# Kernel optimization log

Hardware: AMD Instinct MI355X
Metric: run time of the kernel (lower is better)

## Reference

```python
import jax, jax.numpy as jnp
import numpy as np
import math

NUM_HEADS = 8
HEAD_DIM = 64
SEQ = 128
EPS = 1e-6


def _rel_pos_bucket(rel_pos, num_buckets=32, max_dist=128):
    # bidirectional T5 bucketing
    n = -rel_pos
    num_buckets //= 2  # 16
    ret = (n < 0).astype(jnp.int32) * num_buckets
    n = jnp.abs(n)
    max_exact = num_buckets // 2  # 8
    is_small = n < max_exact
    nf = jnp.maximum(n, 1).astype(jnp.float32)  # guard log(0); masked by is_small
    val_if_large = max_exact + (
        jnp.log(nf / max_exact) / math.log(max_dist / max_exact) * (num_buckets - max_exact)
    ).astype(jnp.int32)
    val_if_large = jnp.minimum(val_if_large, num_buckets - 1)
    return ret + jnp.where(is_small, n, val_if_large)


def setup_inputs() -> dict:
    key = jax.random.key(0)
    ks = jax.random.split(key, 8)
    d = 512
    return {
        "x": jax.random.randint(ks[0], (1, SEQ), 0, 32128),
        "x_len": jax.random.randint(ks[1], (1,), 64, SEQ + 1),
        "embed": jax.random.normal(ks[2], (32128, d), jnp.float32) * 0.02,
        "scale": jnp.ones((d,), jnp.float32),
        "rel_bias_w": jax.random.normal(ks[3], (NUM_HEADS, 32), jnp.float32) * 0.02,
        "qw": jax.random.normal(ks[4], (d, d), jnp.float32) * 0.02,
        "kw": jax.random.normal(ks[5], (d, d), jnp.float32) * 0.02,
        "vw": jax.random.normal(ks[6], (d, d), jnp.float32) * 0.02,
    }


def reference(x, x_len, embed, scale, rel_bias_w, qw, kw, vw):
    B, S = x.shape  # (1, 128)
    H, D = NUM_HEADS, HEAD_DIM

    # embedding gather + RMSNorm + length mask
    h = embed[x]  # [B,S,512]
    var = jnp.mean(jnp.square(h), axis=-1, keepdims=True)
    h = h * jax.lax.rsqrt(var + EPS) * scale
    mask = (jnp.arange(S) < x_len[:, None]).astype(h.dtype)  # [B,S]
    h = h * mask[..., None]

    # relative-position bias gather [H,S,S]
    pos = jnp.arange(S, dtype=jnp.int32)
    rp_bucket = _rel_pos_bucket(pos[:, None] - pos[None, :])  # [S,S]
    rel_bias = rel_bias_w[:, rp_bucket]  # [H,S,S]
    rel_bias = rel_bias + (1.0 - mask[..., None]) * -1e9  # B==1 broadcast

    def split_heads(e):
        # [B,S,512] -> [B*H,S,D]
        return e.reshape(B, S, H, D).transpose(0, 2, 1, 3).reshape(B * H, S, D)

    q = split_heads(h @ qw)
    k = split_heads(h @ kw)
    v = split_heads(h @ vw)

    attn_weights = jnp.einsum("hqd,hkd->hqk", q, k)  # [B*H,S,S]
    attn_weights = attn_weights + jnp.transpose(rel_bias, (0, 2, 1))
    attn_probs = jax.nn.softmax(attn_weights, axis=-1)
    attn_output = jnp.einsum("hqk,hkd->hqd", attn_probs, v)  # [B*H,S,D]
    return (rel_bias, attn_weights, attn_output)
```

## Files before the change

kernel.cpp:

```cpp
#include <hip/hip_runtime.h>

#define SEQL 128
#define DM   512
#define NH   8
#define HD   64

typedef unsigned short ushort_t;
typedef unsigned int   uint_t;
typedef __attribute__((ext_vector_type(8))) __bf16 bf16x8;
typedef __attribute__((ext_vector_type(4))) float  f32x4;

__device__ __forceinline__ ushort_t f2bf(float f) {
    uint_t u = __float_as_uint(f);
    u += 0x7fffu + ((u >> 16) & 1u);
    return (ushort_t)(u >> 16);
}

__device__ __forceinline__ int rel_bucket(int i, int j) {
    int n = j - i;
    int ret = 0;
    if (n < 0) { ret = 16; n = -n; }
    if (n < 8) return ret + n;
    float nf = (float)n;
    int vil = 8 + (int)((logf(nf * 0.125f) / logf(16.0f)) * 8.0f);
    vil = vil < 15 ? vil : 15;
    return ret + vil;
}

__global__ __launch_bounds__(256) void k_qkv_fused(
    const int* __restrict__ x, const int* __restrict__ xlen,
    const float* __restrict__ embed, const float* __restrict__ scale,
    const float* __restrict__ qw, const float* __restrict__ kw,
    const float* __restrict__ vw,
    float* __restrict__ q, float* __restrict__ k, float* __restrict__ v) {
    __shared__ ushort_t Ash[64 * 512];
    __shared__ ushort_t Bsh[2][64 * 64];
    const int t  = threadIdx.x;
    const int n0 = blockIdx.x * 64;
    const int m0 = blockIdx.y * 64;
    const int wi = blockIdx.z;
    const float* __restrict__ W = (wi == 0) ? qw : (wi == 1) ? kw : vw;
    float* __restrict__ O       = (wi == 0) ? q  : (wi == 1) ? k  : v;
    const int xl = xlen[0];

    const int nloc = t & 63, khq = t >> 6;
    const float* __restrict__ wcol = W + n0 + nloc;
    float rc[16];
#pragma unroll
    for (int i = 0; i < 16; ++i) rc[i] = wcol[(size_t)(khq * 16 + i) * DM];

    const int lane7 = t & 7;
#pragma unroll
    for (int p = 0; p < 2; ++p) {
        const int mloc = p * 32 + (t >> 3);
        const int m    = m0 + mloc;
        const int tok  = x[m];
        const float4* er4 = reinterpret_cast<const float4*>(embed + (size_t)tok * DM);
        float4 va[8], vb[8];
#pragma unroll
        for (int j = 0; j < 8; ++j) {
            va[j] = er4[lane7 * 2 + j * 16];
            vb[j] = er4[lane7 * 2 + j * 16 + 1];
        }
        float ss = 0.0f;
#pragma unroll
        for (int j = 0; j < 8; ++j) {
            ss += va[j].x * va[j].x + va[j].y * va[j].y + va[j].z * va[j].z + va[j].w * va[j].w;
            ss += vb[j].x * vb[j].x + vb[j].y * vb[j].y + vb[j].z * vb[j].z + vb[j].w * vb[j].w;
        }
        ss += __shfl_xor(ss, 1);
        ss += __shfl_xor(ss, 2);
        ss += __shfl_xor(ss, 4);
        float inv = rsqrtf(ss * (1.0f / DM) + 1e-6f);
        if (m >= xl) inv = 0.0f;
        const float4* sc4 = reinterpret_cast<const float4*>(scale);
#pragma unroll
        for (int j = 0; j < 8; ++j) {
            const int c = lane7 + 8 * j;
            const float4 s0 = sc4[c * 2];
            const float4 s1 = sc4[c * 2 + 1];
            ushort_t u[8];
            u[0] = f2bf(va[j].x * inv * s0.x);  u[1] = f2bf(va[j].y * inv * s0.y);
            u[2] = f2bf(va[j].z * inv * s0.z);  u[3] = f2bf(va[j].w * inv * s0.w);
            u[4] = f2bf(vb[j].x * inv * s1.x);  u[5] = f2bf(vb[j].y * inv * s1.y);
            u[6] = f2bf(vb[j].z * inv * s1.z);  u[7] = f2bf(vb[j].w * inv * s1.w);
            *reinterpret_cast<uint4*>((char*)Ash + mloc * 1024 + ((c ^ (mloc & 7)) << 4)) =
                *reinterpret_cast<const uint4*>(u);
        }
    }

    {
        ushort_t u[16];
#pragma unroll
        for (int i = 0; i < 16; ++i) u[i] = f2bf(rc[i]);
        char* base = (char*)Bsh + nloc * 128;
        *reinterpret_cast<uint4*>(base + (((khq * 2 + 0) ^ (nloc & 7)) << 4)) =
            *reinterpret_cast<const uint4*>(&u[0]);
        *reinterpret_cast<uint4*>(base + (((khq * 2 + 1) ^ (nloc & 7)) << 4)) =
            *reinterpret_cast<const uint4*>(&u[8]);
    }
#pragma unroll
    for (int i = 0; i < 16; ++i) rc[i] = wcol[(size_t)(64 + khq * 16 + i) * DM];
    __syncthreads();

    const int wid = t >> 6, lane = t & 63;
    const int wm = wid >> 1, wn = wid & 1;
    const int g = lane >> 4, l15 = lane & 15;
    f32x4 acc[2][2] = {};

#pragma unroll
    for (int it = 0; it < 8; ++it) {
        bf16x8 af[2][2], bfr[2][2];
#pragma unroll
        for (int fm = 0; fm < 2; ++fm) {
            const int ml = wm * 32 + fm * 16 + l15;
#pragma unroll
            for (int kh = 0; kh < 2; ++kh) {
                const int c = it * 8 + kh * 4 + g;
                af[fm][kh] = *reinterpret_cast<const bf16x8*>(
                    (const char*)Ash + ml * 1024 + ((c ^ (ml & 7)) << 4));
            }
        }
#pragma unroll
        for (int fn = 0; fn < 2; ++fn) {
            const int nl = wn * 32 + fn * 16 + l15;
#pragma unroll
            for (int kh = 0; kh < 2; ++kh) {
                const int c = kh * 4 + g;
                bfr[fn][kh] = *reinterpret_cast<const bf16x8*>(
                    (const char*)Bsh + (it & 1) * 8192 + nl * 128 + ((c ^ (nl & 7)) << 4));
            }
        }
#pragma unroll
        for (int kh = 0; kh < 2; ++kh)
#pragma unroll
            for (int fm = 0; fm < 2; ++fm)
#pragma unroll
                for (int fn = 0; fn < 2; ++fn)
                    acc[fm][fn] = __builtin_amdgcn_mfma_f32_16x16x32_bf16(
                        af[fm][kh], bfr[fn][kh], acc[fm][fn], 0, 0, 0);

        if (it < 7) {
            ushort_t u[16];
#pragma unroll
            for (int i = 0; i < 16; ++i) u[i] = f2bf(rc[i]);
            char* base = (char*)Bsh + ((it + 1) & 1) * 8192 + nloc * 128;
            *reinterpret_cast<uint4*>(base + (((khq * 2 + 0) ^ (nloc & 7)) << 4)) =
                *reinterpret_cast<const uint4*>(&u[0]);
            *reinterpret_cast<uint4*>(base + (((khq * 2 + 1) ^ (nloc & 7)) << 4)) =
                *reinterpret_cast<const uint4*>(&u[8]);
            if (it < 6) {
#pragma unroll
                for (int i = 0; i < 16; ++i)
                    rc[i] = wcol[(size_t)((it + 2) * 64 + khq * 16 + i) * DM];
            }
        }
        __syncthreads();
    }

#pragma unroll
    for (int fm = 0; fm < 2; ++fm)
#pragma unroll
        for (int fn = 0; fn < 2; ++fn) {
            const int nn = n0 + wn * 32 + fn * 16 + l15;
            float* od = O + ((size_t)(nn >> 6) * SEQL) * HD + (nn & 63);
#pragma unroll
            for (int r = 0; r < 4; ++r) {
                const int mm = m0 + wm * 32 + fm * 16 + g * 4 + r;
                od[(size_t)mm * HD] = acc[fm][fn][r];
            }
        }
}

__global__ __launch_bounds__(256) void k_attn(
    const float* __restrict__ q, const float* __restrict__ k,
    const float* __restrict__ v, const int* __restrict__ xlen,
    const float* __restrict__ rbw,
    float* __restrict__ relb, float* __restrict__ aw, float* __restrict__ ao) {
    const int hh = blockIdx.x;
    const int q0 = blockIdx.y * 4;
    __shared__ float Ks[SEQL][HD + 4];
    __shared__ float ps[4][SEQL];
    const int tid = threadIdx.x;
    const float* __restrict__ kb = k + (size_t)hh * SEQL * HD;
    const float* __restrict__ vb = v + (size_t)hh * SEQL * HD;
    const float4* kb4 = reinterpret_cast<const float4*>(kb);
#pragma unroll
    for (int i = 0; i < 8; ++i) {
        const int e4 = tid + i * 256;
        const float4 kv = kb4[e4];
        *reinterpret_cast<float4*>(&Ks[e4 >> 4][(e4 & 15) * 4]) = kv;
    }
    const int w = tid >> 6, lane = tid & 63;
    const int qi = q0 + w;
    const float4* qrow4 = reinterpret_cast<const float4*>(q + (size_t)(hh * SEQL + qi) * HD);
    float4 qr[16];
#pragma unroll
    for (int i = 0; i < 16; ++i) qr[i] = qrow4[i];
    __syncthreads();
    const int xl = xlen[0];
    float lg[2];
#pragma unroll
    for (int p = 0; p < 2; ++p) {
        const int kk = lane + p * 64;
        float acc = 0.0f;
#pragma unroll
        for (int d4 = 0; d4 < 16; ++d4) {
            const float4 kv = *reinterpret_cast<const float4*>(&Ks[kk][d4 * 4]);
            acc += qr[d4].x * kv.x + qr[d4].y * kv.y + qr[d4].z * kv.z + qr[d4].w * kv.w;
        }
        float bias = rbw[hh * 32 + rel_bucket(kk, qi)];
        if (kk >= xl) bias += -1e9f;
        relb[hh * SEQL * SEQL + kk * SEQL + qi] = bias;
        acc += bias;
        lg[p] = acc;
        aw[hh * SEQL * SEQL + qi * SEQL + kk] = acc;
    }
    float mx = fmaxf(lg[0], lg[1]);
#pragma unroll
    for (int o = 32; o > 0; o >>= 1) mx = fmaxf(mx, __shfl_xor(mx, o));
    const float e0 = expf(lg[0] - mx);
    const float e1 = expf(lg[1] - mx);
    float sm = e0 + e1;
#pragma unroll
    for (int o = 32; o > 0; o >>= 1) sm += __shfl_xor(sm, o);
    const float inv = 1.0f / sm;
    ps[w][lane]      = e0 * inv;
    ps[w][lane + 64] = e1 * inv;
    __syncthreads();
    float accv = 0.0f;
#pragma unroll 8
    for (int kk4 = 0; kk4 < 32; ++kk4) {
        const float4 p4 = *reinterpret_cast<const float4*>(&ps[w][kk4 * 4]);
        accv += p4.x * vb[(kk4 * 4 + 0) * HD + lane]
              + p4.y * vb[(kk4 * 4 + 1) * HD + lane]
              + p4.z * vb[(kk4 * 4 + 2) * HD + lane]
              + p4.w * vb[(kk4 * 4 + 3) * HD + lane];
    }
    ao[(size_t)(hh * SEQL + qi) * HD + lane] = accv;
}

extern "C" void kernel_launch(void* const* d_in, const int* in_sizes, int n_in,
                              void* d_out, int out_size, void* d_ws, size_t ws_size,
                              hipStream_t stream) {
    const int*   x     = (const int*)d_in[0];
    const int*   xlen  = (const int*)d_in[1];
    const float* embed = (const float*)d_in[2];
    const float* scale = (const float*)d_in[3];
    const float* rbw   = (const float*)d_in[4];
    const float* qw    = (const float*)d_in[5];
    const float* kw    = (const float*)d_in[6];
    const float* vw    = (const float*)d_in[7];

    float* out  = (float*)d_out;
    float* relb = out;
    float* aw   = out + NH * SEQL * SEQL;
    float* ao   = out + 2 * NH * SEQL * SEQL;

    float* ws = (float*)d_ws;
    float* q  = ws;
    float* k  = q + SEQL * DM;
    float* v  = k + SEQL * DM;

    k_qkv_fused<<<dim3(8, 2, 3), 256, 0, stream>>>(x, xlen, embed, scale, qw, kw, vw, q, k, v);
    k_attn<<<dim3(NH, SEQL / 4), 256, 0, stream>>>(q, k, v, xlen, rbw, relb, aw, ao);
}
```

Before: 18.14 us.

## Fuse QKV projection and attention into one persistent kernel with flag sync

Result: slower. 36.01 us (+98.5%).

```diff
diff --git a/kernel.cpp b/kernel.cpp
--- a/kernel.cpp
+++ b/kernel.cpp
@@ -27,46 +27,48 @@
     return ret + vil;
 }
 
-__global__ __launch_bounds__(256) void k_qkv_fused(
+__global__ __launch_bounds__(256) void k_fused(
     const int* __restrict__ x, const int* __restrict__ xlen,
     const float* __restrict__ embed, const float* __restrict__ scale,
+    const float* __restrict__ rbw,
     const float* __restrict__ qw, const float* __restrict__ kw,
     const float* __restrict__ vw,
-    float* __restrict__ q, float* __restrict__ k, float* __restrict__ v) {
-    __shared__ ushort_t Ash[64 * 512];
-    __shared__ ushort_t Bsh[2][64 * 64];
-    const int t  = threadIdx.x;
-    const int n0 = blockIdx.x * 64;
-    const int m0 = blockIdx.y * 64;
-    const int wi = blockIdx.z;
-    const float* __restrict__ W = (wi == 0) ? qw : (wi == 1) ? kw : vw;
-    float* __restrict__ O       = (wi == 0) ? q  : (wi == 1) ? k  : v;
+    float* __restrict__ q, float* __restrict__ k, float* __restrict__ v,
+    int* __restrict__ flags,
+    float* __restrict__ relb, float* __restrict__ aw, float* __restrict__ ao) {
+    __shared__ char smem[49152];
+    const int b = blockIdx.x, t = threadIdx.x;
     const int xl = xlen[0];
 
-    const int nloc = t & 63, khq = t >> 6;
-    const float* __restrict__ wcol = W + n0 + nloc;
-    float rc[16];
-#pragma unroll
-    for (int i = 0; i < 16; ++i) rc[i] = wcol[(size_t)(khq * 16 + i) * DM];
-
-    const int lane7 = t & 7;
-#pragma unroll
-    for (int p = 0; p < 2; ++p) {
-        const int mloc = p * 32 + (t >> 3);
-        const int m    = m0 + mloc;
-        const int tok  = x[m];
+    if (b < 96) {
+        ushort_t* Ash = (ushort_t*)smem;
+        ushort_t* Bsh = (ushort_t*)(smem + 32768);
+        const int xb = b & 7, yb = (b >> 3) & 3, zb = b >> 5;
+        const int n0 = xb * 64, m0 = yb * 32;
+        const float* __restrict__ W = (zb == 0) ? qw : (zb == 1) ? kw : vw;
+        float* __restrict__ O       = (zb == 0) ? q  : (zb == 1) ? k  : v;
+
+        const int nloc = t & 63, khq = t >> 6;
+        const float* __restrict__ wcol = W + n0 + nloc;
+        float rc[16];
+#pragma unroll
+        for (int i = 0; i < 16; ++i) rc[i] = wcol[(size_t)(khq * 16 + i) * DM];
+
+        const int lane7 = t & 7, mloc = t >> 3;
+        const int m = m0 + mloc;
+        const int tok = x[m];
         const float4* er4 = reinterpret_cast<const float4*>(embed + (size_t)tok * DM);
-        float4 va[8], vb[8];
+        float4 va[8], vb8[8];
 #pragma unroll
         for (int j = 0; j < 8; ++j) {
-            va[j] = er4[lane7 * 2 + j * 16];
-            vb[j] = er4[lane7 * 2 + j * 16 + 1];
+            va[j]  = er4[lane7 * 2 + j * 16];
+            vb8[j] = er4[lane7 * 2 + j * 16 + 1];
         }
         float ss = 0.0f;
 #pragma unroll
         for (int j = 0; j < 8; ++j) {
             ss += va[j].x * va[j].x + va[j].y * va[j].y + va[j].z * va[j].z + va[j].w * va[j].w;
-            ss += vb[j].x * vb[j].x + vb[j].y * vb[j].y + vb[j].z * vb[j].z + vb[j].w * vb[j].w;
+            ss += vb8[j].x * vb8[j].x + vb8[j].y * vb8[j].y + vb8[j].z * vb8[j].z + vb8[j].w * vb8[j].w;
         }
         ss += __shfl_xor(ss, 1);
         ss += __shfl_xor(ss, 2);
@@ -82,162 +84,193 @@
             ushort_t u[8];
             u[0] = f2bf(va[j].x * inv * s0.x);  u[1] = f2bf(va[j].y * inv * s0.y);
             u[2] = f2bf(va[j].z * inv * s0.z);  u[3] = f2bf(va[j].w * inv * s0.w);
-            u[4] = f2bf(vb[j].x * inv * s1.x);  u[5] = f2bf(vb[j].y * inv * s1.y);
-            u[6] = f2bf(vb[j].z * inv * s1.z);  u[7] = f2bf(vb[j].w * inv * s1.w);
+            u[4] = f2bf(vb8[j].x * inv * s1.x); u[5] = f2bf(vb8[j].y * inv * s1.y);
+            u[6] = f2bf(vb8[j].z * inv * s1.z); u[7] = f2bf(vb8[j].w * inv * s1.w);
             *reinterpret_cast<uint4*>((char*)Ash + mloc * 1024 + ((c ^ (mloc & 7)) << 4)) =
                 *reinterpret_cast<const uint4*>(u);
         }
-    }
-
-    {
-        ushort_t u[16];
-#pragma unroll
-        for (int i = 0; i < 16; ++i) u[i] = f2bf(rc[i]);
-        char* base = (char*)Bsh + nloc * 128;
-        *reinterpret_cast<uint4*>(base + (((khq * 2 + 0) ^ (nloc & 7)) << 4)) =
-            *reinterpret_cast<const uint4*>(&u[0]);
-        *reinterpret_cast<uint4*>(base + (((khq * 2 + 1) ^ (nloc & 7)) << 4)) =
-            *reinterpret_cast<const uint4*>(&u[8]);
-    }
-#pragma unroll
-    for (int i = 0; i < 16; ++i) rc[i] = wcol[(size_t)(64 + khq * 16 + i) * DM];
-    __syncthreads();
-
-    const int wid = t >> 6, lane = t & 63;
-    const int wm = wid >> 1, wn = wid & 1;
-    const int g = lane >> 4, l15 = lane & 15;
-    f32x4 acc[2][2] = {};
-
-#pragma unroll
-    for (int it = 0; it < 8; ++it) {
-        bf16x8 af[2][2], bfr[2][2];
-#pragma unroll
-        for (int fm = 0; fm < 2; ++fm) {
-            const int ml = wm * 32 + fm * 16 + l15;
-#pragma unroll
-            for (int kh = 0; kh < 2; ++kh) {
-                const int c = it * 8 + kh * 4 + g;
-                af[fm][kh] = *reinterpret_cast<const bf16x8*>(
-                    (const char*)Ash + ml * 1024 + ((c ^ (ml & 7)) << 4));
-            }
-        }
-#pragma unroll
-        for (int fn = 0; fn < 2; ++fn) {
-            const int nl = wn * 32 + fn * 16 + l15;
-#pragma unroll
-            for (int kh = 0; kh < 2; ++kh) {
-                const int c = kh * 4 + g;
-                bfr[fn][kh] = *reinterpret_cast<const bf16x8*>(
-                    (const char*)Bsh + (it & 1) * 8192 + nl * 128 + ((c ^ (nl & 7)) << 4));
-            }
-        }
-#pragma unroll
-        for (int kh = 0; kh < 2; ++kh)
-#pragma unroll
-            for (int fm = 0; fm < 2; ++fm)
-#pragma unroll
-                for (int fn = 0; fn < 2; ++fn)
-                    acc[fm][fn] = __builtin_amdgcn_mfma_f32_16x16x32_bf16(
-                        af[fm][kh], bfr[fn][kh], acc[fm][fn], 0, 0, 0);
-
-        if (it < 7) {
+
+        {
             ushort_t u[16];
 #pragma unroll
             for (int i = 0; i < 16; ++i) u[i] = f2bf(rc[i]);
-            char* base = (char*)Bsh + ((it + 1) & 1) * 8192 + nloc * 128;
+            char* base = (char*)Bsh + nloc * 128;
             *reinterpret_cast<uint4*>(base + (((khq * 2 + 0) ^ (nloc & 7)) << 4)) =
                 *reinterpret_cast<const uint4*>(&u[0]);
             *reinterpret_cast<uint4*>(base + (((khq * 2 + 1) ^ (nloc & 7)) << 4)) =
                 *reinterpret_cast<const uint4*>(&u[8]);
-            if (it < 6) {
-#pragma unroll
-                for (int i = 0; i < 16; ++i)
-                    rc[i] = wcol[(size_t)((it + 2) * 64 + khq * 16 + i) * DM];
-            }
-        }
+        }
+#pragma unroll
+        for (int i = 0; i < 16; ++i) rc[i] = wcol[(size_t)(64 + khq * 16 + i) * DM];
         __syncthreads();
+
+        const int wn = t >> 6, lane = t & 63;
+        const int g = lane >> 4, l15 = lane & 15;
+        f32x4 acc[2] = {};
+
+#pragma unroll
+        for (int it = 0; it < 8; ++it) {
+            bf16x8 af[2][2], bfr[2];
+#pragma unroll
+            for (int fm = 0; fm < 2; ++fm) {
+                const int ml = fm * 16 + l15;
+#pragma unroll
+                for (int kh = 0; kh < 2; ++kh) {
+                    const int c = it * 8 + kh * 4 + g;
+                    af[fm][kh] = *reinterpret_cast<const bf16x8*>(
+                        (const char*)Ash + ml * 1024 + ((c ^ (ml & 7)) << 4));
+                }
+            }
+            {
+                const int nl = wn * 16 + l15;
+#pragma unroll
+                for (int kh = 0; kh < 2; ++kh) {
+                    const int c = kh * 4 + g;
+                    bfr[kh] = *reinterpret_cast<const bf16x8*>(
+                        (const char*)Bsh + (it & 1) * 8192 + nl * 128 + ((c ^ (nl & 7)) << 4));
+                }
+            }
+#pragma unroll
+            for (int kh = 0; kh < 2; ++kh)
+#pragma unroll
+                for (int fm = 0; fm < 2; ++fm)
+                    acc[fm] = __builtin_amdgcn_mfma_f32_16x16x32_bf16(
+                        af[fm][kh], bfr[kh], acc[fm], 0, 0, 0);
+
+            if (it < 7) {
+                ushort_t u[16];
+#pragma unroll
+                for (int i = 0; i < 16; ++i) u[i] = f2bf(rc[i]);
+                char* base = (char*)Bsh + ((it + 1) & 1) * 8192 + nloc * 128;
+                *reinterpret_cast<uint4*>(base + (((khq * 2 + 0) ^ (nloc & 7)) << 4)) =
+                    *reinterpret_cast<const uint4*>(&u[0]);
+                *reinterpret_cast<uint4*>(base + (((khq * 2 + 1) ^ (nloc & 7)) << 4)) =
+                    *reinterpret_cast<const uint4*>(&u[8]);
+                if (it < 6) {
+#pragma unroll
+                    for (int i = 0; i < 16; ++i)
+                        rc[i] = wcol[(size_t)((it + 2) * 64 + khq * 16 + i) * DM];
+                }
+            }
+            __syncthreads();
+        }
+
+        {
+            const int nn = n0 + wn * 16 + l15;
+            float* od = O + ((size_t)(nn >> 6) * SEQL) * HD + (nn & 63);
+#pragma unroll
+            for (int fm = 0; fm < 2; ++fm)
+#pragma unroll
+                for (int r = 0; r < 4; ++r) {
+                    const int mm = m0 + fm * 16 + g * 4 + r;
+                    od[(size_t)mm * HD] = acc[fm][r];
+                }
+        }
+        __syncthreads();
+        if (t == 0)
+            __hip_atomic_store(&flags[b], 1, __ATOMIC_RELEASE, __HIP_MEMORY_SCOPE_AGENT);
+    } else {
+        float (*Ks)[HD + 4] = (float(*)[HD + 4])smem;
+        float (*qs)[HD]     = (float(*)[HD])(smem + 34816);
+        float (*ps)[20]     = (float(*)[20])(smem + 38912);
+        const int a = b - 96, hh = a >> 3, qg = a & 7, q0 = qg * 16;
+
+#pragma unroll
+        for (int j = 0; j < 8; ++j) {
+            const int kkr = qg * 16 + j * 2 + (t >> 7);
+            const int qi  = t & 127;
+            float bias = rbw[hh * 32 + rel_bucket(kkr, qi)];
+            if (kkr >= xl) bias += -1e9f;
+            relb[(size_t)hh * SEQL * SEQL + kkr * SEQL + qi] = bias;
+        }
+
+        if (t < 9) {
+            const int fi = (t == 0) ? ((q0 >> 5) * 8 + hh)
+                         : (t < 5)  ? (32 + (t - 1) * 8 + hh)
+                                    : (64 + (t - 5) * 8 + hh);
+            while (__hip_atomic_load(&flags[fi], __ATOMIC_ACQUIRE,
+                                     __HIP_MEMORY_SCOPE_AGENT) == 0)
+                __builtin_amdgcn_s_sleep(2);
+        }
+        __syncthreads();
+        __threadfence();
+
+        const float* __restrict__ kb  = k + (size_t)hh * SEQL * HD;
+        const float* __restrict__ vbp = v + (size_t)hh * SEQL * HD;
+        const float4* kb4 = reinterpret_cast<const float4*>(kb);
+#pragma unroll
+        for (int i = 0; i < 8; ++i) {
+            const int e4 = t + i * 256;
+            *reinterpret_cast<float4*>(&Ks[e4 >> 4][(e4 & 15) * 4]) = kb4[e4];
+        }
+        {
+            const int row = t >> 4, c = (t & 15) * 4;
+            *reinterpret_cast<float4*>(&qs[row][c]) =
+                *reinterpret_cast<const float4*>(q + (size_t)(hh * SEQL + q0 + row) * HD + c);
+        }
+        __syncthreads();
+
+        const int w = t >> 6, lane = t & 63;
+        float lg[2][4];
+#pragma unroll
+        for (int p = 0; p < 2; ++p) {
+            const int kk = lane + p * 64;
+            float accq[4] = {};
+#pragma unroll
+            for (int d4 = 0; d4 < 16; ++d4) {
+                const float4 kv = *reinterpret_cast<const float4*>(&Ks[kk][d4 * 4]);
+#pragma unroll
+                for (int j = 0; j < 4; ++j) {
+                    const float4 qv = *reinterpret_cast<const float4*>(&qs[w * 4 + j][d4 * 4]);
+                    accq[j] += qv.x * kv.x + qv.y * kv.y + qv.z * kv.z + qv.w * kv.w;
+                }
+            }
+#pragma unroll
+            for (int j = 0; j < 4; ++j) {
+                const int qi = q0 + w * 4 + j;
+                float bias = rbw[hh * 32 + rel_bucket(kk, qi)];
+                if (kk >= xl) bias += -1e9f;
+                const float logit = accq[j] + bias;
+                aw[(size_t)hh * SEQL * SEQL + qi * SEQL + kk] = logit;
+                lg[p][j] = logit;
+            }
+        }
+        float pv0[4], pv1[4];
+#pragma unroll
+        for (int j = 0; j < 4; ++j) {
+            float mx = fmaxf(lg[0][j], lg[1][j]);
+#pragma unroll
+            for (int o = 32; o > 0; o >>= 1) mx = fmaxf(mx, __shfl_xor(mx, o));
+            const float e0 = expf(lg[0][j] - mx);
+            const float e1 = expf(lg[1][j] - mx);
+            float sm = e0 + e1;
+#pragma unroll
+            for (int o = 32; o > 0; o >>= 1) sm += __shfl_xor(sm, o);
+            const float inv = 1.0f / sm;
+            pv0[j] = e0 * inv;
+            pv1[j] = e1 * inv;
+        }
+        *reinterpret_cast<float4*>(&ps[lane][w * 4])      = make_float4(pv0[0], pv0[1], pv0[2], pv0[3]);
+        *reinterpret_cast<float4*>(&ps[lane + 64][w * 4]) = make_float4(pv1[0], pv1[1], pv1[2], pv1[3]);
+        float acco[4] = {};
+#pragma unroll
+        for (int kk4 = 0; kk4 < 8; ++kk4) {
+            float vvv[16];
+#pragma unroll
+            for (int u = 0; u < 16; ++u) vvv[u] = vbp[(kk4 * 16 + u) * HD + lane];
+#pragma unroll
+            for (int u = 0; u < 16; ++u) {
+                const float4 pj = *reinterpret_cast<const float4*>(&ps[kk4 * 16 + u][w * 4]);
+                acco[0] += pj.x * vvv[u];
+                acco[1] += pj.y * vvv[u];
+                acco[2] += pj.z * vvv[u];
+                acco[3] += pj.w * vvv[u];
+            }
+        }
+#pragma unroll
+        for (int j = 0; j < 4; ++j)
+            ao[(size_t)(hh * SEQL + q0 + w * 4 + j) * HD + lane] = acco[j];
     }
-
-#pragma unroll
-    for (int fm = 0; fm < 2; ++fm)
-#pragma unroll
-        for (int fn = 0; fn < 2; ++fn) {
-            const int nn = n0 + wn * 32 + fn * 16 + l15;
-            float* od = O + ((size_t)(nn >> 6) * SEQL) * HD + (nn & 63);
-#pragma unroll
-            for (int r = 0; r < 4; ++r) {
-                const int mm = m0 + wm * 32 + fm * 16 + g * 4 + r;
-                od[(size_t)mm * HD] = acc[fm][fn][r];
-            }
-        }
-}
-
-__global__ __launch_bounds__(256) void k_attn(
-    const float* __restrict__ q, const float* __restrict__ k,
-    const float* __restrict__ v, const int* __restrict__ xlen,
-    const float* __restrict__ rbw,
-    float* __restrict__ relb, float* __restrict__ aw, float* __restrict__ ao) {
-    const int hh = blockIdx.x;
-    const int q0 = blockIdx.y * 4;
-    __shared__ float Ks[SEQL][HD + 4];
-    __shared__ float ps[4][SEQL];
-    const int tid = threadIdx.x;
-    const float* __restrict__ kb = k + (size_t)hh * SEQL * HD;
-    const float* __restrict__ vb = v + (size_t)hh * SEQL * HD;
-    const float4* kb4 = reinterpret_cast<const float4*>(kb);
-#pragma unroll
-    for (int i = 0; i < 8; ++i) {
-        const int e4 = tid + i * 256;
-        const float4 kv = kb4[e4];
-        *reinterpret_cast<float4*>(&Ks[e4 >> 4][(e4 & 15) * 4]) = kv;
-    }
-    const int w = tid >> 6, lane = tid & 63;
-    const int qi = q0 + w;
-    const float4* qrow4 = reinterpret_cast<const float4*>(q + (size_t)(hh * SEQL + qi) * HD);
-    float4 qr[16];
-#pragma unroll
-    for (int i = 0; i < 16; ++i) qr[i] = qrow4[i];
-    __syncthreads();
-    const int xl = xlen[0];
-    float lg[2];
-#pragma unroll
-    for (int p = 0; p < 2; ++p) {
-        const int kk = lane + p * 64;
-        float acc = 0.0f;
-#pragma unroll
-        for (int d4 = 0; d4 < 16; ++d4) {
-            const float4 kv = *reinterpret_cast<const float4*>(&Ks[kk][d4 * 4]);
-            acc += qr[d4].x * kv.x + qr[d4].y * kv.y + qr[d4].z * kv.z + qr[d4].w * kv.w;
-        }
-        float bias = rbw[hh * 32 + rel_bucket(kk, qi)];
-        if (kk >= xl) bias += -1e9f;
-        relb[hh * SEQL * SEQL + kk * SEQL + qi] = bias;
-        acc += bias;
-        lg[p] = acc;
-        aw[hh * SEQL * SEQL + qi * SEQL + kk] = acc;
-    }
-    float mx = fmaxf(lg[0], lg[1]);
-#pragma unroll
-    for (int o = 32; o > 0; o >>= 1) mx = fmaxf(mx, __shfl_xor(mx, o));
-    const float e0 = expf(lg[0] - mx);
-    const float e1 = expf(lg[1] - mx);
-    float sm = e0 + e1;
-#pragma unroll
-    for (int o = 32; o > 0; o >>= 1) sm += __shfl_xor(sm, o);
-    const float inv = 1.0f / sm;
-    ps[w][lane]      = e0 * inv;
-    ps[w][lane + 64] = e1 * inv;
-    __syncthreads();
-    float accv = 0.0f;
-#pragma unroll 8
-    for (int kk4 = 0; kk4 < 32; ++kk4) {
-        const float4 p4 = *reinterpret_cast<const float4*>(&ps[w][kk4 * 4]);
-        accv += p4.x * vb[(kk4 * 4 + 0) * HD + lane]
-              + p4.y * vb[(kk4 * 4 + 1) * HD + lane]
-              + p4.z * vb[(kk4 * 4 + 2) * HD + lane]
-              + p4.w * vb[(kk4 * 4 + 3) * HD + lane];
-    }
-    ao[(size_t)(hh * SEQL + qi) * HD + lane] = accv;
 }
 
 extern "C" void kernel_launch(void* const* d_in, const int* in_sizes, int n_in,
@@ -261,7 +294,9 @@
     float* q  = ws;
     float* k  = q + SEQL * DM;
     float* v  = k + SEQL * DM;
-
-    k_qkv_fused<<<dim3(8, 2, 3), 256, 0, stream>>>(x, xlen, embed, scale, qw, kw, vw, q, k, v);
-    k_attn<<<dim3(NH, SEQL / 4), 256, 0, stream>>>(q, k, v, xlen, rbw, relb, aw, ao);
+    int* flags = (int*)(v + SEQL * DM);
+
+    hipMemsetAsync(flags, 0, 96 * sizeof(int), stream);
+    k_fused<<<160, 256, 0, stream>>>(x, xlen, embed, scale, rbw, qw, kw, vw,
+                                     q, k, v, flags, relb, aw, ao);
 }
```

## Move rel-bias output to extra QKV blocks and use per-head bias lookup table

Applied to the files above, without the earlier changes.

Result: no change. 18.37 us (+1.3%).

```diff
diff --git a/kernel.cpp b/kernel.cpp
--- a/kernel.cpp
+++ b/kernel.cpp
@@ -16,8 +16,8 @@
     return (ushort_t)(u >> 16);
 }
 
-__device__ __forceinline__ int rel_bucket(int i, int j) {
-    int n = j - i;
+__device__ __forceinline__ int bucket_of_delta(int d) {
+    int n = d;
     int ret = 0;
     if (n < 0) { ret = 16; n = -n; }
     if (n < 8) return ret + n;
@@ -27,21 +27,41 @@
     return ret + vil;
 }
 
-__global__ __launch_bounds__(256) void k_qkv_fused(
+__global__ __launch_bounds__(256) void k_qkv_relb(
     const int* __restrict__ x, const int* __restrict__ xlen,
     const float* __restrict__ embed, const float* __restrict__ scale,
+    const float* __restrict__ rbw,
     const float* __restrict__ qw, const float* __restrict__ kw,
     const float* __restrict__ vw,
-    float* __restrict__ q, float* __restrict__ k, float* __restrict__ v) {
-    __shared__ ushort_t Ash[64 * 512];
-    __shared__ ushort_t Bsh[2][64 * 64];
+    float* __restrict__ q, float* __restrict__ k, float* __restrict__ v,
+    float* __restrict__ relb) {
+    __shared__ char smem[81920];
     const int t  = threadIdx.x;
+    const int zb = blockIdx.z;
+    const int xl = xlen[0];
+
+    if (zb == 3) {
+        float* tbl = (float*)smem;
+        const int hh = blockIdx.x, half = blockIdx.y;
+        if (t < 255) tbl[t] = rbw[hh * 32 + bucket_of_delta(t - 127)];
+        __syncthreads();
+        const int qi = t & 127, kkoff = t >> 7;
+#pragma unroll
+        for (int j = 0; j < 32; ++j) {
+            const int kk = half * 64 + j * 2 + kkoff;
+            float bias = tbl[qi - kk + 127];
+            if (kk >= xl) bias += -1e9f;
+            relb[(size_t)hh * SEQL * SEQL + kk * SEQL + qi] = bias;
+        }
+        return;
+    }
+
+    ushort_t* Ash = (ushort_t*)smem;
+    ushort_t* Bsh = (ushort_t*)(smem + 65536);
     const int n0 = blockIdx.x * 64;
     const int m0 = blockIdx.y * 64;
-    const int wi = blockIdx.z;
-    const float* __restrict__ W = (wi == 0) ? qw : (wi == 1) ? kw : vw;
-    float* __restrict__ O       = (wi == 0) ? q  : (wi == 1) ? k  : v;
-    const int xl = xlen[0];
+    const float* __restrict__ W = (zb == 0) ? qw : (zb == 1) ? kw : vw;
+    float* __restrict__ O       = (zb == 0) ? q  : (zb == 1) ? k  : v;
 
     const int nloc = t & 63, khq = t >> 6;
     const float* __restrict__ wcol = W + n0 + nloc;
@@ -56,17 +76,17 @@
         const int m    = m0 + mloc;
         const int tok  = x[m];
         const float4* er4 = reinterpret_cast<const float4*>(embed + (size_t)tok * DM);
-        float4 va[8], vb[8];
+        float4 va[8], vb8[8];
 #pragma unroll
         for (int j = 0; j < 8; ++j) {
-            va[j] = er4[lane7 * 2 + j * 16];
-            vb[j] = er4[lane7 * 2 + j * 16 + 1];
+            va[j]  = er4[lane7 * 2 + j * 16];
+            vb8[j] = er4[lane7 * 2 + j * 16 + 1];
         }
         float ss = 0.0f;
 #pragma unroll
         for (int j = 0; j < 8; ++j) {
             ss += va[j].x * va[j].x + va[j].y * va[j].y + va[j].z * va[j].z + va[j].w * va[j].w;
-            ss += vb[j].x * vb[j].x + vb[j].y * vb[j].y + vb[j].z * vb[j].z + vb[j].w * vb[j].w;
+            ss += vb8[j].x * vb8[j].x + vb8[j].y * vb8[j].y + vb8[j].z * vb8[j].z + vb8[j].w * vb8[j].w;
         }
         ss += __shfl_xor(ss, 1);
         ss += __shfl_xor(ss, 2);
@@ -82,8 +102,8 @@
             ushort_t u[8];
             u[0] = f2bf(va[j].x * inv * s0.x);  u[1] = f2bf(va[j].y * inv * s0.y);
             u[2] = f2bf(va[j].z * inv * s0.z);  u[3] = f2bf(va[j].w * inv * s0.w);
-            u[4] = f2bf(vb[j].x * inv * s1.x);  u[5] = f2bf(vb[j].y * inv * s1.y);
-            u[6] = f2bf(vb[j].z * inv * s1.z);  u[7] = f2bf(vb[j].w * inv * s1.w);
+            u[4] = f2bf(vb8[j].x * inv * s1.x); u[5] = f2bf(vb8[j].y * inv * s1.y);
+            u[6] = f2bf(vb8[j].z * inv * s1.z); u[7] = f2bf(vb8[j].w * inv * s1.w);
             *reinterpret_cast<uint4*>((char*)Ash + mloc * 1024 + ((c ^ (mloc & 7)) << 4)) =
                 *reinterpret_cast<const uint4*>(u);
         }
@@ -172,15 +192,16 @@
         }
 }
 
-__global__ __launch_bounds__(256) void k_attn(
+__global__ __launch_bounds__(256) void k_attn4(
     const float* __restrict__ q, const float* __restrict__ k,
     const float* __restrict__ v, const int* __restrict__ xlen,
     const float* __restrict__ rbw,
-    float* __restrict__ relb, float* __restrict__ aw, float* __restrict__ ao) {
+    float* __restrict__ aw, float* __restrict__ ao) {
     const int hh = blockIdx.x;
     const int q0 = blockIdx.y * 4;
     __shared__ float Ks[SEQL][HD + 4];
     __shared__ float ps[4][SEQL];
+    __shared__ float tbl[255];
     const int tid = threadIdx.x;
     const float* __restrict__ kb = k + (size_t)hh * SEQL * HD;
     const float* __restrict__ vb = v + (size_t)hh * SEQL * HD;
@@ -188,8 +209,7 @@
 #pragma unroll
     for (int i = 0; i < 8; ++i) {
         const int e4 = tid + i * 256;
-        const float4 kv = kb4[e4];
-        *reinterpret_cast<float4*>(&Ks[e4 >> 4][(e4 & 15) * 4]) = kv;
+        *reinterpret_cast<float4*>(&Ks[e4 >> 4][(e4 & 15) * 4]) = kb4[e4];
     }
     const int w = tid >> 6, lane = tid & 63;
     const int qi = q0 + w;
@@ -197,6 +217,7 @@
     float4 qr[16];
 #pragma unroll
     for (int i = 0; i < 16; ++i) qr[i] = qrow4[i];
+    if (tid < 255) tbl[tid] = rbw[hh * 32 + bucket_of_delta(tid - 127)];
     __syncthreads();
     const int xl = xlen[0];
     float lg[2];
@@ -209,9 +230,8 @@
             const float4 kv = *reinterpret_cast<const float4*>(&Ks[kk][d4 * 4]);
             acc += qr[d4].x * kv.x + qr[d4].y * kv.y + qr[d4].z * kv.z + qr[d4].w * kv.w;
         }
-        float bias = rbw[hh * 32 + rel_bucket(kk, qi)];
+        float bias = tbl[qi - kk + 127];
         if (kk >= xl) bias += -1e9f;
-        relb[hh * SEQL * SEQL + kk * SEQL + qi] = bias;
         acc += bias;
         lg[p] = acc;
         aw[hh * SEQL * SEQL + qi * SEQL + kk] = acc;
@@ -227,7 +247,6 @@
     const float inv = 1.0f / sm;
     ps[w][lane]      = e0 * inv;
     ps[w][lane + 64] = e1 * inv;
-    __syncthreads();
     float accv = 0.0f;
 #pragma unroll 8
     for (int kk4 = 0; kk4 < 32; ++kk4) {
@@ -262,6 +281,7 @@
     float* k  = q + SEQL * DM;
     float* v  = k + SEQL * DM;
 
-    k_qkv_fused<<<dim3(8, 2, 3), 256, 0, stream>>>(x, xlen, embed, scale, qw, kw, vw, q, k, v);
-    k_attn<<<dim3(NH, SEQL / 4), 256, 0, stream>>>(q, k, v, xlen, rbw, relb, aw, ao);
-}
+    k_qkv_relb<<<dim3(8, 2, 4), 256, 0, stream>>>(x, xlen, embed, scale, rbw,
+                                                  qw, kw, vw, q, k, v, relb);
+    k_attn4<<<dim3(NH, SEQL / 4), 256, 0, stream>>>(q, k, v, xlen, rbw, aw, ao);
+}
```
